# Kernel optimization log

Measured on AMD Instinct MI355X. Metric: run time of the kernel, lower is better.

Reference implementation:

```python
import jax, jax.numpy as jnp
import numpy as np

B, N, E, H = 16, 1024, 1024, 16  # batch must equal num_heads due to the 'hbkd' einsum in the original
D = E // H


def setup_inputs() -> dict:
    key = jax.random.key(0)
    ks = jax.random.split(key, 9)
    s = 0.02
    return {
        "x": jax.random.normal(ks[0], (B, N, E), dtype=jnp.float32),
        "Wq": jax.random.normal(ks[1], (E, E), dtype=jnp.float32) * s,
        "bq": jax.random.normal(ks[2], (E,), dtype=jnp.float32) * s,
        "Wk": jax.random.normal(ks[3], (E, E), dtype=jnp.float32) * s,
        "bk": jax.random.normal(ks[4], (E,), dtype=jnp.float32) * s,
        "Wv": jax.random.normal(ks[5], (E, E), dtype=jnp.float32) * s,
        "bv": jax.random.normal(ks[6], (E,), dtype=jnp.float32) * s,
        "Wp": jax.random.normal(ks[7], (E, E), dtype=jnp.float32) * s,
        "bp": jax.random.normal(ks[8], (E,), dtype=jnp.float32) * s,
    }


def _split_heads(t):  # [b, n, (h d)] -> [b, h, n, d]
    b, n, e = t.shape
    return t.reshape(b, n, H, D).transpose(0, 2, 1, 3)


def reference(x, Wq, bq, Wk, bk, Wv, bv, Wp, bp):
    q = _split_heads(x @ Wq.T + bq)  # [b, h, n, d]
    k = _split_heads(x @ Wk.T + bk)
    v = _split_heads(x @ Wv.T + bv)
    # Faithful to original: K is contracted with its batch/head axes SWAPPED ('hbkd').
    energy = jnp.einsum('bhqd,hbkd->bhqk', q, k)  # [b, h, n, n]
    # Faithful: softmax over the HEAD axis (dim=1), scale applied AFTER softmax.
    scale = E ** 0.5
    att = jax.nn.softmax(energy, axis=1) / scale
    # dropout rate is 0.0 -> identity
    o = jnp.einsum('bhal,bhlv->bhav', att, v)  # [b, h, n, d]
    o = o.transpose(0, 2, 1, 3).reshape(B, N, E)  # [b, n, (h d)]
    return o @ Wp.T + bp
```

## Files before the change

kernel.cpp:

```cpp
#include <hip/hip_runtime.h>
#include <hip/hip_bf16.h>

#define DEVI __device__ __forceinline__

typedef float f32x4 __attribute__((ext_vector_type(4)));
typedef short bf16x8 __attribute__((ext_vector_type(8)));
typedef unsigned short u16x4 __attribute__((ext_vector_type(4)));


DEVI unsigned short f2bf(float f) {
  union { float f; unsigned u; } v; v.f = f;
  unsigned r = v.u + 0x7fffu + ((v.u >> 16) & 1u);
  return (unsigned short)(r >> 16);
}

DEVI float fexp2(float x) {
#if __has_builtin(__builtin_amdgcn_exp2f)
  return __builtin_amdgcn_exp2f(x);
#else
  return exp2f(x);
#endif
}

DEVI float frcp(float x) {
#if __has_builtin(__builtin_amdgcn_rcpf)
  return __builtin_amdgcn_rcpf(x);
#else
  return 1.0f / x;
#endif
}

DEVI unsigned cvtpk(float a, float b) {
  unsigned r;
  asm("v_cvt_pk_bf16_f32 %0, %1, %2" : "=v"(r) : "v"(a), "v"(b));
  return r;
}

DEVI void gload_lds16(const unsigned short* g, unsigned short* l) {
  __builtin_amdgcn_global_load_lds(
      (const __attribute__((address_space(1))) void*)g,
      (__attribute__((address_space(3))) void*)l, 16, 0, 0);
}

DEVI void wg_barrier() {
  asm volatile("s_waitcnt lgkmcnt(0)" ::: "memory");
  __builtin_amdgcn_s_barrier();
  __builtin_amdgcn_sched_barrier(0);
}

__global__ void cvt_kernel(const float* __restrict__ s, unsigned short* __restrict__ d, int n4) {
  int i = blockIdx.x * blockDim.x + threadIdx.x;
  const int st = gridDim.x * blockDim.x;
  for (; i < n4; i += st) {
    const float4 v = reinterpret_cast<const float4*>(s)[i];
    u16x4 o;
    o[0] = f2bf(v.x); o[1] = f2bf(v.y); o[2] = f2bf(v.z); o[3] = f2bf(v.w);
    reinterpret_cast<u16x4*>(d)[i] = o;
  }
}


#define STA(BUF, C, K0) gload_lds16(&A[(size_t)(m0 + (C)*64 + srow) * 1024 + (K0) + scol], &lsA[BUF][(C)*4096 + tid*8])
#define STB(BUF, C, K0) gload_lds16(&Bw[(size_t)(n0 + (C)*64 + srow) * 1024 + (K0) + scol], &lsB[BUF][(C)*4096 + tid*8])

#define DSREAD_A(BUF, MF, KS) (*(const bf16x8*)&lsA[BUF][arow + (MF)*1024 + ((KS) ? sx1 : sx0)])
#define DSREAD_B(BUF, NF, KS) (*(const bf16x8*)&lsB[BUF][brow + (NF)*1024 + ((KS) ? sx1 : sx0)])

#define MFMA16(P, AF)                                                          \
    __builtin_amdgcn_s_setprio(1);                                             \
    _Pragma("unroll") for (int mfi = 0; mfi < 2; mfi++)                        \
      _Pragma("unroll") for (int nf = 0; nf < 4; nf++)                         \
        _Pragma("unroll") for (int ks = 0; ks < 2; ks++)                       \
          acc[2*(P)+mfi][nf] = __builtin_amdgcn_mfma_f32_16x16x32_bf16(        \
              AF[mfi][ks], bfr[nf][ks], acc[2*(P)+mfi][nf], 0, 0, 0);          \
    __builtin_amdgcn_s_setprio(0);

#define PHASE(BUF, P, LB, STG)                                                 \
  { __builtin_amdgcn_s_barrier();                                              \
    bf16x8 af[2][2];                                                           \
    _Pragma("unroll") for (int i = 0; i < 2; i++)                              \
      _Pragma("unroll") for (int k2 = 0; k2 < 2; k2++)                         \
        af[i][k2] = DSREAD_A(BUF, 2*(P)+i, k2);                                \
    if (LB) {                                                                  \
      _Pragma("unroll") for (int n2 = 0; n2 < 4; n2++)                         \
        _Pragma("unroll") for (int k2 = 0; k2 < 2; k2++)                       \
          bfr[n2][k2] = DSREAD_B(BUF, n2, k2);                                 \
    }                                                                          \
    STG;                                                                       \
    MFMA16(P, af) }

#define GSTEP(CB, NB, K1)                                                      \
    asm volatile("s_waitcnt vmcnt(2)" ::: "memory");                           \
    PHASE(CB, 0, 1, { STB(NB,0,K1); STB(NB,1,K1); })                           \
    PHASE(CB, 1, 0, { STB(NB,2,K1); STB(NB,3,K1); })                           \
    asm volatile("s_waitcnt vmcnt(4)" ::: "memory");                           \
    PHASE(CB, 2, 0, { STA(NB,0,K1); STA(NB,2,K1); })                           \
    PHASE(CB, 3, 0, { STA(NB,1,K1); STA(NB,3,K1); })

DEVI void gemm256_main(const unsigned short* __restrict__ A,
                       const unsigned short* __restrict__ Bw,
                       int m0, int n0,
                       unsigned short (&lsA)[2][16384],
                       unsigned short (&lsB)[2][16384],
                       f32x4 (&acc)[8][4]) {
  const int tid = threadIdx.x;
  const int l = tid & 63, lr = l & 15, lg = l >> 4;
  const int w = tid >> 6, wm = w >> 2, wn = w & 3;
  const int srow = tid >> 3;
  const int scol = (((tid & 7) ^ (srow & 7)) * 8);
  const int sx0 = (lg * 8) ^ ((lr & 7) << 3);
  const int sx1 = (32 + lg * 8) ^ ((lr & 7) << 3);
  const int arow = (wm * 128 + lr) * 64;
  const int brow = (wn * 64 + lr) * 64;

  STB(0,0,0); STB(0,1,0); STB(0,2,0); STB(0,3,0);
  STA(0,0,0); STA(0,1,0); STA(0,2,0); STA(0,3,0);
  asm volatile("s_waitcnt vmcnt(0)" ::: "memory");
  __builtin_amdgcn_s_barrier();

  bf16x8 bfr[4][2];

#pragma unroll 1
  for (int t7 = 0; t7 < 7; ++t7) {
    const int k1 = t7 * 128 + 64;
    GSTEP(0, 1, k1)
    GSTEP(1, 0, k1 + 64)
  }
  GSTEP(0, 1, 960)
  asm volatile("s_waitcnt vmcnt(2)" ::: "memory");
  PHASE(1, 0, 1, {})
  PHASE(1, 1, 0, {})
  asm volatile("s_waitcnt vmcnt(0)" ::: "memory");
  PHASE(1, 2, 0, {})
  PHASE(1, 3, 0, {})
}

__global__ __launch_bounds__(512, 2) void proj_qkv8(
    const unsigned short* __restrict__ A, const unsigned short* __restrict__ W3,
    const float* __restrict__ bq, const float* __restrict__ bk, const float* __restrict__ bv,
    unsigned short* __restrict__ outq, unsigned short* __restrict__ outk, unsigned short* __restrict__ outv) {
  __shared__ unsigned short lsA[2][16384];
  __shared__ unsigned short lsB[2][16384];
  const int z = blockIdx.z;
  const int m0 = blockIdx.x * 256, n0 = blockIdx.y * 256;
  const unsigned short* Bw = W3 + z * 1048576;
  f32x4 acc[8][4];
  const f32x4 z4 = {0.f, 0.f, 0.f, 0.f};
#pragma unroll
  for (int i = 0; i < 8; i++)
#pragma unroll
    for (int j = 0; j < 4; j++) acc[i][j] = z4;

  gemm256_main(A, Bw, m0, n0, lsA, lsB, acc);

  const int tid = threadIdx.x;
  const int l = tid & 63, lr = l & 15, lg = l >> 4;
  const int w = tid >> 6, wm = w >> 2, wn = w & 3;
  const float* bias = (z == 0) ? bq : ((z == 1) ? bk : bv);
  const float SC = 1.4426950408889634f;
#pragma unroll
  for (int mf = 0; mf < 8; mf++) {
    const int mb = m0 + wm * 128 + mf * 16 + lg * 4;
#pragma unroll
    for (int nf = 0; nf < 4; nf++) {
      const int ncol = n0 + wn * 64 + nf * 16 + lr;
      const float bsv = bias[ncol];
      const int h = ncol >> 6, d = ncol & 63;
      if (z == 0) {
        const int ks = d >> 5, lgq = (d >> 3) & 3, eq = d & 7;
#pragma unroll
        for (int r = 0; r < 4; r++) {
          const int m = mb + r;
          const int bb = m >> 10, nr = m & 1023;
          const int nt = nr >> 4, lrq = nr & 15;
          const int idx = (((bb * 64 + nt) * 32 + h * 2 + ks) * 64 + lgq * 16 + lrq) * 8 + eq;
          outq[idx] = f2bf((acc[mf][nf][r] + bsv) * SC);
        }
      } else if (z == 1) {
        const int ks = d >> 5, lhi = ((d >> 3) & 3) * 16, eq = d & 7;
#pragma unroll
        for (int r = 0; r < 4; r++) {
          const int m = mb + r;
          const int n = m & 1023, bx = m >> 10;
          const int lane = lhi + (n & 15);
          const int idx = ((((h * 64 + (n >> 4)) * 16 + bx) * 2 + ks) * 64 + lane) * 8 + eq;
          outk[idx] = f2bf(acc[mf][nf][r] + bsv);
        }
      } else {
        const int dt = d >> 4, lrv = d & 15;
        const int bb = mb >> 10, n = mb & 1023;
        const int kc = n >> 5, lgv = (n >> 3) & 3, ev = n & 7;
        u16x4 pk;
#pragma unroll
        for (int r = 0; r < 4; r++) pk[r] = f2bf(acc[mf][nf][r] + bsv);
        const int idx0 = ((((bb * 16 + h) * 32 + kc) * 4 + dt) * 64 + lgv * 16 + lrv) * 8 + ev;
        *(u16x4*)&outv[idx0] = pk;
      }
    }
  }
}

__global__ __launch_bounds__(512, 2) void proj_out8(
    const unsigned short* __restrict__ A, const unsigned short* __restrict__ Wp,
    const float* __restrict__ bias, float* __restrict__ out) {
  __shared__ unsigned short lsA[2][16384];
  __shared__ unsigned short lsB[2][16384];
  const int m0 = blockIdx.x * 256, n0 = blockIdx.y * 256;
  f32x4 acc[8][4];
  const f32x4 z4 = {0.f, 0.f, 0.f, 0.f};
#pragma unroll
  for (int i = 0; i < 8; i++)
#pragma unroll
    for (int j = 0; j < 4; j++) acc[i][j] = z4;

  gemm256_main(A, Wp, m0, n0, lsA, lsB, acc);

  const int tid = threadIdx.x;
  const int l = tid & 63, lr = l & 15, lg = l >> 4;
  const int w = tid >> 6, wm = w >> 2, wn = w & 3;
#pragma unroll
  for (int mf = 0; mf < 8; mf++) {
    const int mb = m0 + wm * 128 + mf * 16 + lg * 4;
#pragma unroll
    for (int nf = 0; nf < 4; nf++) {
      const int ncol = n0 + wn * 64 + nf * 16 + lr;
      const float bsv = bias[ncol];
#pragma unroll
      for (int r = 0; r < 4; r++) out[(size_t)(mb + r) * 1024 + ncol] = acc[mf][nf][r] + bsv;
    }
  }
}

#define ATTN_BODY(IT, KC, KN)                                                  \
  {                                                                            \
    int qo = 0;                                                                \
    asm volatile("" : "+v"(qo));                                               \
    f32x4 e[4][2];                                                             \
    _Pragma("unroll") for (int hl = 0; hl < 4; hl++) {                         \
      const int h = hq * 4 + hl;                                               \
      _Pragma("unroll") for (int qh = 0; qh < 2; qh++) {                       \
        bf16x8 q0 = *(const bf16x8*)((const char*)qlds + qo + (qh * 32 + h * 2 + 0) * 1024 + l * 16); \
        bf16x8 q1 = *(const bf16x8*)((const char*)qlds + qo + (qh * 32 + h * 2 + 1) * 1024 + l * 16); \
        f32x4 t = __builtin_amdgcn_mfma_f32_16x16x32_bf16(KC[hl * 2 + 0], q0, z4, 0, 0, 0); \
        t = __builtin_amdgcn_mfma_f32_16x16x32_bf16(KC[hl * 2 + 1], q1, t, 0, 0, 0); \
        t[0] = fexp2(t[0]); t[1] = fexp2(t[1]); t[2] = fexp2(t[2]); t[3] = fexp2(t[3]); \
        e[hl][qh] = t;                                                         \
      }                                                                        \
    }                                                                          \
    {                                                                          \
      const unsigned short* knp = kroot + (size_t)((((IT) + 1) & 15) * 4) * 16384; \
      _Pragma("unroll") for (int i = 0; i < 8; i++) KN[i] = *(const bf16x8*)(knp + i * 512); \
    }                                                                          \
    f32x4 s0 = (e[0][0] + e[1][0]) + (e[2][0] + e[3][0]);                      \
    f32x4 s1 = (e[0][1] + e[1][1]) + (e[2][1] + e[3][1]);                      \
    *(f32x4*)&sumbuf[((ksub * 4 + hq) * 2 + 0) * 256 + l * 4] = s0;            \
    *(f32x4*)&sumbuf[((ksub * 4 + hq) * 2 + 1) * 256 + l * 4] = s1;            \
    wg_barrier();                                                              \
    _Pragma("unroll") for (int p = 1; p < 4; p++) {                            \
      const int hqp = hq ^ p;                                                  \
      s0 += *(const f32x4*)&sumbuf[((ksub * 4 + hqp) * 2 + 0) * 256 + l * 4];  \
      s1 += *(const f32x4*)&sumbuf[((ksub * 4 + hqp) * 2 + 1) * 256 + l * 4];  \
    }                                                                          \
    f32x4 inv0, inv1;                                                          \
    inv0[0] = frcp(s0[0]) * 0.03125f; inv0[1] = frcp(s0[1]) * 0.03125f;        \
    inv0[2] = frcp(s0[2]) * 0.03125f; inv0[3] = frcp(s0[3]) * 0.03125f;        \
    inv1[0] = frcp(s1[0]) * 0.03125f; inv1[1] = frcp(s1[1]) * 0.03125f;        \
    inv1[2] = frcp(s1[2]) * 0.03125f; inv1[3] = frcp(s1[3]) * 0.03125f;        \
    _Pragma("unroll") for (int hl = 0; hl < 4; hl++) {                         \
      const int h = hq * 4 + hl;                                               \
      _Pragma("unroll") for (int qh = 0; qh < 2; qh++) {                       \
        f32x4 vv = e[hl][qh] * (qh ? inv1 : inv0);                             \
        uint2 pk;                                                              \
        pk.x = cvtpk(vv[0], vv[1]);                                            \
        pk.y = cvtpk(vv[2], vv[3]);                                            \
        *(uint2*)((char*)abuf + h * 4096 + (qh * 16 + lr) * 128 + ((kpart ^ wswz) << 1)) = pk; \
      }                                                                        \
    }                                                                          \
    {                                                                          \
      const unsigned short* vbp = vroot + (size_t)((IT) * 2) * 2048;           \
      _Pragma("unroll") for (int kst = 0; kst < 2; kst++)                      \
        _Pragma("unroll") for (int dt = 0; dt < 4; dt++)                       \
          vr[kst * 4 + dt] = *(const bf16x8*)(vbp + kst * 2048 + dt * 512);    \
    }                                                                          \
    wg_barrier();                                                              \
    bf16x8 pa[2][2];                                                           \
    _Pragma("unroll") for (int qt = 0; qt < 2; qt++)                           \
      _Pragma("unroll") for (int kst = 0; kst < 2; kst++)                      \
        pa[qt][kst] = *(const bf16x8*)((const char*)abuf + w * 4096 + qt * 2048 + lr * 128 + (((kst * 4 + lg) ^ (lr & 7)) << 4)); \
    _Pragma("unroll") for (int qt = 0; qt < 2; qt++)                           \
      _Pragma("unroll") for (int kst = 0; kst < 2; kst++)                      \
        _Pragma("unroll") for (int dt = 0; dt < 4; dt++)                       \
          oacc[qt][dt] = __builtin_amdgcn_mfma_f32_16x16x32_bf16(pa[qt][kst], vr[kst * 4 + dt], oacc[qt][dt], 0, 0, 0); \
  }

__global__ __launch_bounds__(1024, 4) void attn5(
    const unsigned short* __restrict__ Q2,
    const unsigned short* __restrict__ K2,
    const unsigned short* __restrict__ V2,
    unsigned short* __restrict__ O) {
  __shared__ unsigned short qlds[32768];
  __shared__ unsigned short abuf[32768];
  __shared__ float sumbuf[8192];

  const int tid = threadIdx.x;
  const int w = tid >> 6, l = tid & 63;
  const int lr = l & 15, lg = l >> 4;
  const int bid = blockIdx.x;
  const int swz = (bid & 7) * 64 + (bid >> 3);
  const int b = swz >> 5, qt32 = swz & 31;
  const int ksub = w & 3, hq = w >> 2;

  {
    const unsigned short* qsrc = Q2 + (size_t)(b * 64 + qt32 * 2) * 16384 + tid * 8;
    unsigned short* qdst = qlds + tid * 8;
#pragma unroll
    for (int r = 0; r < 4; r++) gload_lds16(qsrc + r * 8192, qdst + r * 8192);
  }

  const int kpart = ksub * 16 + lg * 4;
  const int wswz = (lr & 7) << 3;

  const f32x4 z4 = {0.f, 0.f, 0.f, 0.f};
  f32x4 oacc[2][4];
#pragma unroll
  for (int qt = 0; qt < 2; qt++)
#pragma unroll
    for (int dt = 0; dt < 4; dt++) oacc[qt][dt] = z4;

  const unsigned short* kroot = K2 + (size_t)(b * 64 + ksub) * 16384 + hq * 4096 + l * 8;
  const unsigned short* vroot = V2 + (size_t)((b * 16 + w) * 32) * 2048 + l * 8;

  bf16x8 kA[8], kB[8], vr[8];
#pragma unroll
  for (int i = 0; i < 8; i++) kA[i] = *(const bf16x8*)(kroot + i * 512);

  asm volatile("s_waitcnt vmcnt(0) lgkmcnt(0)" ::: "memory");
  __builtin_amdgcn_s_barrier();
  __builtin_amdgcn_sched_barrier(0);

#pragma unroll 1
  for (int it2 = 0; it2 < 8; it2++) {
    ATTN_BODY(it2 * 2, kA, kB)
    ATTN_BODY(it2 * 2 + 1, kB, kA)
  }

#pragma unroll
  for (int qt = 0; qt < 2; qt++)
#pragma unroll
    for (int dt = 0; dt < 4; dt++)
#pragma unroll
      for (int r = 0; r < 4; r++) {
        const int n = qt32 * 32 + qt * 16 + lg * 4 + r;
        O[(size_t)(b * 1024 + n) * 1024 + w * 64 + dt * 16 + lr] = f2bf(oacc[qt][dt][r]);
      }
}

extern "C" void kernel_launch(void* const* d_in, const int* in_sizes, int n_in,
                              void* d_out, int out_size, void* d_ws, size_t ws_size,
                              hipStream_t stream) {
  const float* x  = (const float*)d_in[0];
  const float* Wq = (const float*)d_in[1];
  const float* bq = (const float*)d_in[2];
  const float* Wk = (const float*)d_in[3];
  const float* bk = (const float*)d_in[4];
  const float* Wv = (const float*)d_in[5];
  const float* bv = (const float*)d_in[6];
  const float* Wp = (const float*)d_in[7];
  const float* bp = (const float*)d_in[8];

  char* ws = (char*)d_ws;
  unsigned short* xbf  = (unsigned short*)(ws);
  unsigned short* qbf  = (unsigned short*)(ws + 33554432);
  unsigned short* kbf  = (unsigned short*)(ws + 67108864);
  unsigned short* vtbf = (unsigned short*)(ws + 100663296);
  unsigned short* wbf  = (unsigned short*)(ws + 134217728);

  cvt_kernel<<<2048, 256, 0, stream>>>(x, xbf, 4194304);
  cvt_kernel<<<512, 256, 0, stream>>>(Wq, wbf, 262144);
  cvt_kernel<<<512, 256, 0, stream>>>(Wk, wbf + 1048576, 262144);
  cvt_kernel<<<512, 256, 0, stream>>>(Wv, wbf + 2097152, 262144);
  cvt_kernel<<<512, 256, 0, stream>>>(Wp, wbf + 3145728, 262144);

  proj_qkv8<<<dim3(64, 4, 3), 512, 0, stream>>>(xbf, wbf, bq, bk, bv, qbf, kbf, vtbf);
  attn5<<<512, 1024, 0, stream>>>(qbf, kbf, vtbf, xbf);
  proj_out8<<<dim3(64, 4, 1), 512, 0, stream>>>(xbf, wbf + 3145728, bp, (float*)d_out);
}
```

Measured before the change: 330.7 us.

## Process two key blocks per iteration with LDS-atomic softmax sum reduction

The attention loop now handles two key blocks per iteration. It computes both sets of exp-scores up front and reduces the head-axis softmax sums for both with LDS float atomicAdd into a small shared accumulator, replacing the store/barrier/read-partner exchange. The normalized high block is kept packed in registers and written to the shared buffer only after the low block's PV MFMAs finish, so one sum reduction serves two blocks. The explicit K register double-buffering prefetch is gone and K is loaded just before use, which may expose global-load latency and raise register pressure.

```diff
diff --git a/kernel.cpp b/kernel.cpp
--- a/kernel.cpp
+++ b/kernel.cpp
@@ -58,7 +58,6 @@
     reinterpret_cast<u16x4*>(d)[i] = o;
   }
 }
-
 
 #define STA(BUF, C, K0) gload_lds16(&A[(size_t)(m0 + (C)*64 + srow) * 1024 + (K0) + scol], &lsA[BUF][(C)*4096 + tid*8])
 #define STB(BUF, C, K0) gload_lds16(&Bw[(size_t)(n0 + (C)*64 + srow) * 1024 + (K0) + scol], &lsB[BUF][(C)*4096 + tid*8])
@@ -231,76 +230,14 @@
   }
 }
 
-#define ATTN_BODY(IT, KC, KN)                                                  \
-  {                                                                            \
-    int qo = 0;                                                                \
-    asm volatile("" : "+v"(qo));                                               \
-    f32x4 e[4][2];                                                             \
-    _Pragma("unroll") for (int hl = 0; hl < 4; hl++) {                         \
-      const int h = hq * 4 + hl;                                               \
-      _Pragma("unroll") for (int qh = 0; qh < 2; qh++) {                       \
-        bf16x8 q0 = *(const bf16x8*)((const char*)qlds + qo + (qh * 32 + h * 2 + 0) * 1024 + l * 16); \
-        bf16x8 q1 = *(const bf16x8*)((const char*)qlds + qo + (qh * 32 + h * 2 + 1) * 1024 + l * 16); \
-        f32x4 t = __builtin_amdgcn_mfma_f32_16x16x32_bf16(KC[hl * 2 + 0], q0, z4, 0, 0, 0); \
-        t = __builtin_amdgcn_mfma_f32_16x16x32_bf16(KC[hl * 2 + 1], q1, t, 0, 0, 0); \
-        t[0] = fexp2(t[0]); t[1] = fexp2(t[1]); t[2] = fexp2(t[2]); t[3] = fexp2(t[3]); \
-        e[hl][qh] = t;                                                         \
-      }                                                                        \
-    }                                                                          \
-    {                                                                          \
-      const unsigned short* knp = kroot + (size_t)((((IT) + 1) & 15) * 4) * 16384; \
-      _Pragma("unroll") for (int i = 0; i < 8; i++) KN[i] = *(const bf16x8*)(knp + i * 512); \
-    }                                                                          \
-    f32x4 s0 = (e[0][0] + e[1][0]) + (e[2][0] + e[3][0]);                      \
-    f32x4 s1 = (e[0][1] + e[1][1]) + (e[2][1] + e[3][1]);                      \
-    *(f32x4*)&sumbuf[((ksub * 4 + hq) * 2 + 0) * 256 + l * 4] = s0;            \
-    *(f32x4*)&sumbuf[((ksub * 4 + hq) * 2 + 1) * 256 + l * 4] = s1;            \
-    wg_barrier();                                                              \
-    _Pragma("unroll") for (int p = 1; p < 4; p++) {                            \
-      const int hqp = hq ^ p;                                                  \
-      s0 += *(const f32x4*)&sumbuf[((ksub * 4 + hqp) * 2 + 0) * 256 + l * 4];  \
-      s1 += *(const f32x4*)&sumbuf[((ksub * 4 + hqp) * 2 + 1) * 256 + l * 4];  \
-    }                                                                          \
-    f32x4 inv0, inv1;                                                          \
-    inv0[0] = frcp(s0[0]) * 0.03125f; inv0[1] = frcp(s0[1]) * 0.03125f;        \
-    inv0[2] = frcp(s0[2]) * 0.03125f; inv0[3] = frcp(s0[3]) * 0.03125f;        \
-    inv1[0] = frcp(s1[0]) * 0.03125f; inv1[1] = frcp(s1[1]) * 0.03125f;        \
-    inv1[2] = frcp(s1[2]) * 0.03125f; inv1[3] = frcp(s1[3]) * 0.03125f;        \
-    _Pragma("unroll") for (int hl = 0; hl < 4; hl++) {                         \
-      const int h = hq * 4 + hl;                                               \
-      _Pragma("unroll") for (int qh = 0; qh < 2; qh++) {                       \
-        f32x4 vv = e[hl][qh] * (qh ? inv1 : inv0);                             \
-        uint2 pk;                                                              \
-        pk.x = cvtpk(vv[0], vv[1]);                                            \
-        pk.y = cvtpk(vv[2], vv[3]);                                            \
-        *(uint2*)((char*)abuf + h * 4096 + (qh * 16 + lr) * 128 + ((kpart ^ wswz) << 1)) = pk; \
-      }                                                                        \
-    }                                                                          \
-    {                                                                          \
-      const unsigned short* vbp = vroot + (size_t)((IT) * 2) * 2048;           \
-      _Pragma("unroll") for (int kst = 0; kst < 2; kst++)                      \
-        _Pragma("unroll") for (int dt = 0; dt < 4; dt++)                       \
-          vr[kst * 4 + dt] = *(const bf16x8*)(vbp + kst * 2048 + dt * 512);    \
-    }                                                                          \
-    wg_barrier();                                                              \
-    bf16x8 pa[2][2];                                                           \
-    _Pragma("unroll") for (int qt = 0; qt < 2; qt++)                           \
-      _Pragma("unroll") for (int kst = 0; kst < 2; kst++)                      \
-        pa[qt][kst] = *(const bf16x8*)((const char*)abuf + w * 4096 + qt * 2048 + lr * 128 + (((kst * 4 + lg) ^ (lr & 7)) << 4)); \
-    _Pragma("unroll") for (int qt = 0; qt < 2; qt++)                           \
-      _Pragma("unroll") for (int kst = 0; kst < 2; kst++)                      \
-        _Pragma("unroll") for (int dt = 0; dt < 4; dt++)                       \
-          oacc[qt][dt] = __builtin_amdgcn_mfma_f32_16x16x32_bf16(pa[qt][kst], vr[kst * 4 + dt], oacc[qt][dt], 0, 0, 0); \
-  }
-
-__global__ __launch_bounds__(1024, 4) void attn5(
+__global__ __launch_bounds__(1024, 4) void attn9(
     const unsigned short* __restrict__ Q2,
     const unsigned short* __restrict__ K2,
     const unsigned short* __restrict__ V2,
     unsigned short* __restrict__ O) {
   __shared__ unsigned short qlds[32768];
   __shared__ unsigned short abuf[32768];
-  __shared__ float sumbuf[8192];
+  __shared__ float sumacc[16 * 320];
 
   const int tid = threadIdx.x;
   const int w = tid >> 6, l = tid & 63;
@@ -316,9 +253,13 @@
 #pragma unroll
     for (int r = 0; r < 4; r++) gload_lds16(qsrc + r * 8192, qdst + r * 8192);
   }
+#pragma unroll
+  for (int r = 0; r < 4; r++) sumacc[w * 320 + l * 5 + r] = 0.f;
 
   const int kpart = ksub * 16 + lg * 4;
   const int wswz = (lr & 7) << 3;
+  const int t_l0 = (0 * 4 + ksub) * 2 + 0, t_l1 = (0 * 4 + ksub) * 2 + 1;
+  const int t_h0 = (1 * 4 + ksub) * 2 + 0, t_h1 = (1 * 4 + ksub) * 2 + 1;
 
   const f32x4 z4 = {0.f, 0.f, 0.f, 0.f};
   f32x4 oacc[2][4];
@@ -329,19 +270,136 @@
 
   const unsigned short* kroot = K2 + (size_t)(b * 64 + ksub) * 16384 + hq * 4096 + l * 8;
   const unsigned short* vroot = V2 + (size_t)((b * 16 + w) * 32) * 2048 + l * 8;
-
-  bf16x8 kA[8], kB[8], vr[8];
-#pragma unroll
-  for (int i = 0; i < 8; i++) kA[i] = *(const bf16x8*)(kroot + i * 512);
 
   asm volatile("s_waitcnt vmcnt(0) lgkmcnt(0)" ::: "memory");
   __builtin_amdgcn_s_barrier();
   __builtin_amdgcn_sched_barrier(0);
 
 #pragma unroll 1
-  for (int it2 = 0; it2 < 8; it2++) {
-    ATTN_BODY(it2 * 2, kA, kB)
-    ATTN_BODY(it2 * 2 + 1, kB, kA)
+  for (int it = 0; it < 8; it++) {
+    int qo = 0;
+    asm volatile("" : "+v"(qo));
+    const unsigned short* kplo = kroot + (size_t)(it * 8) * 16384;
+    const unsigned short* kphi = kroot + (size_t)(it * 8 + 4) * 16384;
+    const unsigned short* vblo = vroot + (size_t)(it * 4) * 2048;
+    const unsigned short* vbhi = vroot + (size_t)(it * 4 + 2) * 2048;
+
+    f32x4 elo[4][2], ehi[4][2];
+    f32x4 sl0 = z4, sl1 = z4, sh0 = z4, sh1 = z4;
+#pragma unroll
+    for (int hl = 0; hl < 4; hl++) {
+      const int h = hq * 4 + hl;
+      bf16x8 kl0 = *(const bf16x8*)(kplo + (hl * 2 + 0) * 512);
+      bf16x8 kl1 = *(const bf16x8*)(kplo + (hl * 2 + 1) * 512);
+      bf16x8 kh0 = *(const bf16x8*)(kphi + (hl * 2 + 0) * 512);
+      bf16x8 kh1 = *(const bf16x8*)(kphi + (hl * 2 + 1) * 512);
+#pragma unroll
+      for (int qh = 0; qh < 2; qh++) {
+        bf16x8 q0 = *(const bf16x8*)((const char*)qlds + qo + (qh * 32 + h * 2 + 0) * 1024 + l * 16);
+        bf16x8 q1 = *(const bf16x8*)((const char*)qlds + qo + (qh * 32 + h * 2 + 1) * 1024 + l * 16);
+        f32x4 t = __builtin_amdgcn_mfma_f32_16x16x32_bf16(kl0, q0, z4, 0, 0, 0);
+        t = __builtin_amdgcn_mfma_f32_16x16x32_bf16(kl1, q1, t, 0, 0, 0);
+        t[0] = fexp2(t[0]); t[1] = fexp2(t[1]); t[2] = fexp2(t[2]); t[3] = fexp2(t[3]);
+        elo[hl][qh] = t;
+        if (qh) sl1 += t; else sl0 += t;
+        f32x4 u = __builtin_amdgcn_mfma_f32_16x16x32_bf16(kh0, q0, z4, 0, 0, 0);
+        u = __builtin_amdgcn_mfma_f32_16x16x32_bf16(kh1, q1, u, 0, 0, 0);
+        u[0] = fexp2(u[0]); u[1] = fexp2(u[1]); u[2] = fexp2(u[2]); u[3] = fexp2(u[3]);
+        ehi[hl][qh] = u;
+        if (qh) sh1 += u; else sh0 += u;
+      }
+    }
+#pragma unroll
+    for (int r = 0; r < 4; r++) {
+      atomicAdd(&sumacc[t_l0 * 320 + l * 5 + r], sl0[r]);
+      atomicAdd(&sumacc[t_l1 * 320 + l * 5 + r], sl1[r]);
+      atomicAdd(&sumacc[t_h0 * 320 + l * 5 + r], sh0[r]);
+      atomicAdd(&sumacc[t_h1 * 320 + l * 5 + r], sh1[r]);
+    }
+    wg_barrier();
+
+    f32x4 inv_l0, inv_l1, inv_h0, inv_h1;
+#pragma unroll
+    for (int r = 0; r < 4; r++) {
+      inv_l0[r] = frcp(sumacc[t_l0 * 320 + l * 5 + r]) * 0.03125f;
+      inv_l1[r] = frcp(sumacc[t_l1 * 320 + l * 5 + r]) * 0.03125f;
+      inv_h0[r] = frcp(sumacc[t_h0 * 320 + l * 5 + r]) * 0.03125f;
+      inv_h1[r] = frcp(sumacc[t_h1 * 320 + l * 5 + r]) * 0.03125f;
+    }
+    uint2 pkhi[4][2];
+#pragma unroll
+    for (int hl = 0; hl < 4; hl++) {
+      const int h = hq * 4 + hl;
+#pragma unroll
+      for (int qh = 0; qh < 2; qh++) {
+        f32x4 vl = elo[hl][qh] * (qh ? inv_l1 : inv_l0);
+        uint2 pk;
+        pk.x = cvtpk(vl[0], vl[1]);
+        pk.y = cvtpk(vl[2], vl[3]);
+        *(uint2*)((char*)abuf + h * 4096 + (qh * 16 + lr) * 128 + ((kpart ^ wswz) << 1)) = pk;
+        f32x4 vh = ehi[hl][qh] * (qh ? inv_h1 : inv_h0);
+        pkhi[hl][qh].x = cvtpk(vh[0], vh[1]);
+        pkhi[hl][qh].y = cvtpk(vh[2], vh[3]);
+      }
+    }
+    bf16x8 vr0[4], vr1[4];
+#pragma unroll
+    for (int dt = 0; dt < 4; dt++) vr0[dt] = *(const bf16x8*)(vblo + dt * 512);
+    wg_barrier();
+
+#pragma unroll
+    for (int r = 0; r < 4; r++) sumacc[w * 320 + l * 5 + r] = 0.f;
+
+    bf16x8 pa[2][2];
+#pragma unroll
+    for (int qt = 0; qt < 2; qt++)
+#pragma unroll
+      for (int kst = 0; kst < 2; kst++)
+        pa[qt][kst] = *(const bf16x8*)((const char*)abuf + w * 4096 + qt * 2048 + lr * 128 +
+                                       (((kst * 4 + lg) ^ (lr & 7)) << 4));
+#pragma unroll
+    for (int dt = 0; dt < 4; dt++) vr1[dt] = *(const bf16x8*)(vblo + 2048 + dt * 512);
+#pragma unroll
+    for (int qt = 0; qt < 2; qt++)
+#pragma unroll
+      for (int dt = 0; dt < 4; dt++)
+        oacc[qt][dt] = __builtin_amdgcn_mfma_f32_16x16x32_bf16(pa[qt][0], vr0[dt], oacc[qt][dt], 0, 0, 0);
+#pragma unroll
+    for (int qt = 0; qt < 2; qt++)
+#pragma unroll
+      for (int dt = 0; dt < 4; dt++)
+        oacc[qt][dt] = __builtin_amdgcn_mfma_f32_16x16x32_bf16(pa[qt][1], vr1[dt], oacc[qt][dt], 0, 0, 0);
+    wg_barrier();
+
+#pragma unroll
+    for (int hl = 0; hl < 4; hl++) {
+      const int h = hq * 4 + hl;
+#pragma unroll
+      for (int qh = 0; qh < 2; qh++)
+        *(uint2*)((char*)abuf + h * 4096 + (qh * 16 + lr) * 128 + ((kpart ^ wswz) << 1)) = pkhi[hl][qh];
+    }
+#pragma unroll
+    for (int dt = 0; dt < 4; dt++) vr0[dt] = *(const bf16x8*)(vbhi + dt * 512);
+    wg_barrier();
+
+#pragma unroll
+    for (int qt = 0; qt < 2; qt++)
+#pragma unroll
+      for (int kst = 0; kst < 2; kst++)
+        pa[qt][kst] = *(const bf16x8*)((const char*)abuf + w * 4096 + qt * 2048 + lr * 128 +
+                                       (((kst * 4 + lg) ^ (lr & 7)) << 4));
+#pragma unroll
+    for (int dt = 0; dt < 4; dt++) vr1[dt] = *(const bf16x8*)(vbhi + 2048 + dt * 512);
+#pragma unroll
+    for (int qt = 0; qt < 2; qt++)
+#pragma unroll
+      for (int dt = 0; dt < 4; dt++)
+        oacc[qt][dt] = __builtin_amdgcn_mfma_f32_16x16x32_bf16(pa[qt][0], vr0[dt], oacc[qt][dt], 0, 0, 0);
+#pragma unroll
+    for (int qt = 0; qt < 2; qt++)
+#pragma unroll
+      for (int dt = 0; dt < 4; dt++)
+        oacc[qt][dt] = __builtin_amdgcn_mfma_f32_16x16x32_bf16(pa[qt][1], vr1[dt], oacc[qt][dt], 0, 0, 0);
   }
 
 #pragma unroll
@@ -382,6 +440,6 @@
   cvt_kernel<<<512, 256, 0, stream>>>(Wp, wbf + 3145728, 262144);
 
   proj_qkv8<<<dim3(64, 4, 3), 512, 0, stream>>>(xbf, wbf, bq, bk, bv, qbf, kbf, vtbf);
-  attn5<<<512, 1024, 0, stream>>>(qbf, kbf, vtbf, xbf);
+  attn9<<<512, 1024, 0, stream>>>(qbf, kbf, vtbf, xbf);
   proj_out8<<<dim3(64, 4, 1), 512, 0, stream>>>(xbf, wbf + 3145728, bp, (float*)d_out);
 }
```

Measured after the change: 657.9 us. 99.0% more time.
